# Optimization experiments

Measured on AMD Instinct MI355X. Metric: run time of the kernel, lower is better.

## Reference

```python
import jax, jax.numpy as jnp
import numpy as np

B = 4_194_304  # batch size


def _apply_rot(s0, s1, phi, theta, omega):
    """Apply PennyLane Rot(phi,theta,omega) = RZ(omega) RY(theta) RZ(phi) to state (s0,s1).
    Matrix: [[e^{-i(phi+omega)/2} c, -e^{i(phi-omega)/2} s],
             [e^{-i(phi-omega)/2} s,  e^{i(phi+omega)/2} c]] with c=cos(theta/2), s=sin(theta/2).
    """
    c = jnp.cos(theta * 0.5)
    s = jnp.sin(theta * 0.5)
    a = 0.5 * (phi + omega)
    b = 0.5 * (phi - omega)
    ea = jnp.exp(-1j * a)  # e^{-i(phi+omega)/2}
    eb = jnp.exp(1j * b)   # e^{ i(phi-omega)/2}
    m00 = ea * c
    m01 = -eb * s
    m10 = jnp.conj(eb) * s
    m11 = jnp.conj(ea) * c
    return m00 * s0 + m01 * s1, m10 * s0 + m11 * s1


def setup_inputs() -> dict:
    key = jax.random.key(0)
    k1, k2 = jax.random.split(key)
    input_features = jax.random.normal(k1, (B, 12), dtype=jnp.float32)
    weights = jax.random.normal(k2, (24,), dtype=jnp.float32)
    return {"input_features": input_features, "weights": weights}


def reference(input_features, weights):
    x = input_features  # [B, 12]
    w = weights         # [24]
    # angles for gate g, slot j: w[6g+2j] + x[:, 3g+j] * w[6g+2j+1]
    s0 = jnp.ones((x.shape[0],), dtype=jnp.complex64)   # |0> amplitude
    s1 = jnp.zeros((x.shape[0],), dtype=jnp.complex64)
    for g in range(4):
        phi = w[6 * g + 0] + x[:, 3 * g + 0] * w[6 * g + 1]
        theta = w[6 * g + 2] + x[:, 3 * g + 1] * w[6 * g + 3]
        omega = w[6 * g + 4] + x[:, 3 * g + 2] * w[6 * g + 5]
        s0, s1 = _apply_rot(s0, s1, phi, theta, omega)
    # expval of Hermitian [[1,0],[0,0]] = |<0|psi>|^2
    out = jnp.real(s0) ** 2 + jnp.imag(s0) ** 2  # [B]
    return out
```

## Files before the change

### kernel.cpp

```cpp
#include <hip/hip_runtime.h>

__global__ __launch_bounds__(256) void QGN_30219389895238_kernel(
    const float* __restrict__ x,
    const float* __restrict__ w,
    float* __restrict__ out,
    int n) {
  int i = blockIdx.x * blockDim.x + threadIdx.x;
  if (i >= n) return;

  const float4* __restrict__ xr = reinterpret_cast<const float4*>(x + (size_t)i * 12);
  float4 r0 = xr[0];
  float4 r1 = xr[1];
  float4 r2 = xr[2];
  float xv[12] = {r0.x, r0.y, r0.z, r0.w,
                  r1.x, r1.y, r1.z, r1.w,
                  r2.x, r2.y, r2.z, r2.w};

  float s0r = 1.0f, s0i = 0.0f, s1r = 0.0f, s1i = 0.0f;

#pragma unroll
  for (int g = 0; g < 4; ++g) {
    float phi   = w[6 * g + 0] + xv[3 * g + 0] * w[6 * g + 1];
    float theta = w[6 * g + 2] + xv[3 * g + 1] * w[6 * g + 3];
    float omega = w[6 * g + 4] + xv[3 * g + 2] * w[6 * g + 5];

    float s, c;
    __sincosf(theta * 0.5f, &s, &c);
    float a = 0.5f * (phi + omega);
    float b = 0.5f * (phi - omega);
    float sa, ca, sb, cb;
    __sincosf(a, &sa, &ca);
    __sincosf(b, &sb, &cb);

    float m00r =  ca * c, m00i = -sa * c;
    float m01r = -cb * s, m01i = -sb * s;
    float m10r =  cb * s, m10i = -sb * s;
    float m11r =  ca * c, m11i =  sa * c;

    float n0r = m00r * s0r - m00i * s0i + m01r * s1r - m01i * s1i;
    float n0i = m00r * s0i + m00i * s0r + m01r * s1i + m01i * s1r;
    float n1r = m10r * s0r - m10i * s0i + m11r * s1r - m11i * s1i;
    float n1i = m10r * s0i + m10i * s0r + m11r * s1i + m11i * s1r;
    s0r = n0r; s0i = n0i; s1r = n1r; s1i = n1i;
  }

  out[i] = s0r * s0r + s0i * s0i;
}

extern "C" void kernel_launch(void* const* d_in, const int* in_sizes, int n_in,
                              void* d_out, int out_size, void* d_ws, size_t ws_size,
                              hipStream_t stream) {
  const float* x = (const float*)d_in[0];
  const float* w = (const float*)d_in[1];
  float* out = (float*)d_out;
  int n = in_sizes[0] / 12;
  int block = 256;
  int grid = (n + block - 1) / block;
  QGN_30219389895238_kernel<<<grid, block, 0, stream>>>(x, w, out, n);
}
```

Measured before the change: 272.7 us.

## Decompose rotations into merged RZ/RY chain and drop the initial and final phase terms

Rewrites the four Rot gates as an alternating chain of RY and merged RZ rotations, where adjacent RZ(omega_g) and RZ(phi_{g+1}) are combined into one phase. The first RZ(phi) on |0> and the last RZ(omega) only contribute a global phase to the output amplitude, so they are skipped. This reduces the transcendental count from 12 sincos to 7 and cuts the complex matrix arithmetic. The kernel is likely memory-bound (reading 48 bytes per element), so the saved ALU work may matter little.

```diff
diff --git a/kernel.cpp b/kernel.cpp
--- a/kernel.cpp
+++ b/kernel.cpp
@@ -12,39 +12,44 @@
   float4 r0 = xr[0];
   float4 r1 = xr[1];
   float4 r2 = xr[2];
-  float xv[12] = {r0.x, r0.y, r0.z, r0.w,
-                  r1.x, r1.y, r1.z, r1.w,
-                  r2.x, r2.y, r2.z, r2.w};
+  float ht1 = 0.5f * (w[2]  + r0.y * w[3]);
+  float ht2 = 0.5f * (w[8]  + r1.x * w[9]);
+  float ht3 = 0.5f * (w[14] + r1.w * w[15]);
+  float ht4 = 0.5f * (w[20] + r2.z * w[21]);
+  float ha1 = 0.5f * ((w[4]  + r0.z * w[5])  + (w[6]  + r0.w * w[7]));
+  float ha2 = 0.5f * ((w[10] + r1.y * w[11]) + (w[12] + r1.z * w[13]));
+  float ha3 = 0.5f * ((w[16] + r2.x * w[17]) + (w[18] + r2.y * w[19]));
 
-  float s0r = 1.0f, s0i = 0.0f, s1r = 0.0f, s1i = 0.0f;
+  float c1 = __cosf(ht1), n1 = __sinf(ht1);
 
-#pragma unroll
-  for (int g = 0; g < 4; ++g) {
-    float phi   = w[6 * g + 0] + xv[3 * g + 0] * w[6 * g + 1];
-    float theta = w[6 * g + 2] + xv[3 * g + 1] * w[6 * g + 3];
-    float omega = w[6 * g + 4] + xv[3 * g + 2] * w[6 * g + 5];
+  float ca = __cosf(ha1), sa = __sinf(ha1);
+  float s0r = c1 * ca, s0i = -c1 * sa;
+  float s1r = n1 * ca, s1i =  n1 * sa;
 
-    float s, c;
-    __sincosf(theta * 0.5f, &s, &c);
-    float a = 0.5f * (phi + omega);
-    float b = 0.5f * (phi - omega);
-    float sa, ca, sb, cb;
-    __sincosf(a, &sa, &ca);
-    __sincosf(b, &sb, &cb);
+  float c = __cosf(ht2), s = __sinf(ht2);
+  float t0r = c * s0r - s * s1r, t0i = c * s0i - s * s1i;
+  float t1r = s * s0r + c * s1r, t1i = s * s0i + c * s1i;
+  s0r = t0r; s0i = t0i; s1r = t1r; s1i = t1i;
 
-    float m00r =  ca * c, m00i = -sa * c;
-    float m01r = -cb * s, m01i = -sb * s;
-    float m10r =  cb * s, m10i = -sb * s;
-    float m11r =  ca * c, m11i =  sa * c;
+  ca = __cosf(ha2); sa = __sinf(ha2);
+  t0r = s0r * ca + s0i * sa; t0i = s0i * ca - s0r * sa;
+  t1r = s1r * ca - s1i * sa; t1i = s1i * ca + s1r * sa;
+  s0r = t0r; s0i = t0i; s1r = t1r; s1i = t1i;
 
-    float n0r = m00r * s0r - m00i * s0i + m01r * s1r - m01i * s1i;
-    float n0i = m00r * s0i + m00i * s0r + m01r * s1i + m01i * s1r;
-    float n1r = m10r * s0r - m10i * s0i + m11r * s1r - m11i * s1i;
-    float n1i = m10r * s0i + m10i * s0r + m11r * s1i + m11i * s1r;
-    s0r = n0r; s0i = n0i; s1r = n1r; s1i = n1i;
-  }
+  c = __cosf(ht3); s = __sinf(ht3);
+  t0r = c * s0r - s * s1r; t0i = c * s0i - s * s1i;
+  t1r = s * s0r + c * s1r; t1i = s * s0i + c * s1i;
+  s0r = t0r; s0i = t0i; s1r = t1r; s1i = t1i;
 
-  out[i] = s0r * s0r + s0i * s0i;
+  ca = __cosf(ha3); sa = __sinf(ha3);
+  t0r = s0r * ca + s0i * sa; t0i = s0i * ca - s0r * sa;
+  t1r = s1r * ca - s1i * sa; t1i = s1i * ca + s1r * sa;
+  s0r = t0r; s0i = t0i; s1r = t1r; s1i = t1i;
+
+  c = __cosf(ht4); s = __sinf(ht4);
+  t0r = c * s0r - s * s1r; t0i = c * s0i - s * s1i;
+
+  out[i] = t0r * t0r + t0i * t0i;
 }
 
 extern "C" void kernel_launch(void* const* d_in, const int* in_sizes, int n_in,
```

Result: no change. 271.3 us (-0.5%).
